# Optimization experiments

Measured on AMD Instinct MI355X. Metric: run time of the kernel, lower is better.

Reference implementation:

```python
import jax, jax.numpy as jnp
import numpy as np

B, N, DM, H, C, DC = 4, 1024, 512, 8, 3, 16  # batch, nodes, node_dim, heads, manifold components, per-component dim
DK = DM // H


def setup_inputs() -> dict:
    key = jax.random.key(0)
    ks = jax.random.split(key, 8)

    def lin_w(k):
        return jax.random.normal(k, (DM, DM), jnp.float32) / np.sqrt(DM).astype(np.float32)

    return {
        "h": jax.random.normal(ks[0], (B, N, DM), jnp.float32),
        "x": jax.random.normal(ks[1], (B, N, C * DC), jnp.float32),
        "Wq": lin_w(ks[2]), "bq": jnp.zeros((DM,), jnp.float32),
        "Wk": lin_w(ks[3]), "bk": jnp.zeros((DM,), jnp.float32),
        "Wv": lin_w(ks[4]), "bv": jnp.zeros((DM,), jnp.float32),
        "Wo": lin_w(ks[5]), "bo": jnp.zeros((DM,), jnp.float32),
        "alpha": jnp.ones((H, C), jnp.float32),
        "log_sigma": jnp.zeros((H, C), jnp.float32),
    }


def reference(h, x, Wq, bq, Wk, bk, Wv, bv, Wo, bo, alpha, log_sigma):
    b, n, dm = h.shape
    hh, cc = alpha.shape
    dk = dm // hh
    scale = 1.0 / np.sqrt(dk).astype(np.float32)

    def to_heads(t, W, bias):
        return (t @ W.T + bias).reshape(b, n, hh, dk).transpose(0, 2, 1, 3)  # (B,H,N,dk)

    Q = to_heads(h, Wq, bq)
    K = to_heads(h, Wk, bk)
    V = to_heads(h, Wv, bv)

    attn = jnp.einsum('bhid,bhjd->bhij', Q, K) * scale  # (B,H,N,N)

    # Geodesic kernel: per-component Euclidean distances on the product manifold.
    xs = x.reshape(b, n, cc, -1)                      # (B,N,C,dc)
    sq = jnp.sum(xs * xs, axis=-1)                    # (B,N,C)
    inner = jnp.einsum('bicd,bjcd->bijc', xs, xs)     # (B,N,N,C)
    d_sq = jnp.maximum(sq[:, :, None, :] + sq[:, None, :, :] - 2.0 * inner, 0.0)  # (B,N,N,C)

    sigma = jnp.clip(jnp.exp(log_sigma), 1e-4)        # (H,C)
    # exp(-d_c^2 / (2 sigma_{h,c}^2)) -> (B,H,N,N,C), then weight by alpha and sum over c
    e = jnp.exp(-d_sq[:, None] / (2.0 * (sigma ** 2)[None, :, None, None, :])).astype(attn.dtype)
    attn = attn + jnp.einsum('hc,bhijc->bhij', alpha, e)

    p = jax.nn.softmax(attn, axis=-1)
    out = jnp.einsum('bhij,bhjd->bhid', p, V)         # (B,H,N,dk)
    out = out.transpose(0, 2, 1, 3).reshape(b, n, dm)
    return out @ Wo.T + bo
```

## Files before the change

kernel.cpp:

```cpp
#include <hip/hip_runtime.h>
#include <math.h>

typedef __bf16 bf16;
typedef __attribute__((ext_vector_type(8))) __bf16 bf16x8;
typedef __attribute__((ext_vector_type(4))) float f32x4;

#define LOG2E 1.44269504088896f
#define SCALE 0.125f

__device__ inline f32x4 mfma16(bf16x8 a, bf16x8 b, f32x4 c) {
    return __builtin_amdgcn_mfma_f32_16x16x32_bf16(a, b, c, 0, 0, 0);
}
__device__ inline unsigned short bfb(bf16 v) {
    union { bf16 b; unsigned short u; } z; z.b = v; return z.u;
}

__global__ __launch_bounds__(256) void prep_kernel(
        const float* __restrict__ h, const float* __restrict__ x,
        const float* __restrict__ Wq, const float* __restrict__ Wk,
        const float* __restrict__ Wv, const float* __restrict__ Wo,
        const float* __restrict__ bq, const float* __restrict__ bk,
        const float* __restrict__ bv,
        bf16* __restrict__ hb, bf16* __restrict__ wpack, bf16* __restrict__ wob,
        float* __restrict__ bqkv, bf16* __restrict__ xb,
        unsigned* __restrict__ spack) {
    int stride = gridDim.x * blockDim.x;
    int tid = blockIdx.x * blockDim.x + threadIdx.x;
    for (int i = tid; i < 4096 * 512; i += stride) hb[i] = (bf16)h[i];
    for (int i = tid; i < 262144; i += stride) {
        wpack[i]          = (bf16)Wq[i];
        wpack[262144 + i] = (bf16)Wk[i];
        wpack[524288 + i] = (bf16)Wv[i];
    }
    for (int i = tid; i < 512 * 512; i += stride) wob[i] = (bf16)Wo[i];
    for (int i = tid; i < 1536; i += stride)
        bqkv[i] = (i < 512) ? bq[i] : (i < 1024 ? bk[i - 512] : bv[i - 1024]);
    for (int i = tid; i < 4096 * 48; i += stride) xb[i] = (bf16)x[i];
    for (int i = tid; i < 4096 * 3; i += stride) {
        int row = i / 3, c = i - row * 3;
        float s = 0.0f;
        for (int k = 0; k < 16; k++) {
            float v = (float)(bf16)x[row * 48 + c * 16 + k];
            s += v * v;
        }
        s = -0.5f * s;
        bf16 sh = (bf16)s;
        bf16 sl = (bf16)(s - (float)sh);
        spack[i] = (unsigned)bfb(sh) | ((unsigned)bfb(sl) << 16);
    }
}

__global__ __launch_bounds__(256) void gemm_qkv_kernel(
        const bf16* __restrict__ A, const bf16* __restrict__ Bm,
        const float* __restrict__ bias,
        bf16* __restrict__ Qb, bf16* __restrict__ Kb, bf16* __restrict__ Vt) {
    __shared__ bf16 smem[2 * 128 * 72];
    bf16 (*Asm)[72] = (bf16(*)[72])smem;
    bf16 (*Bsm)[72] = (bf16(*)[72])(smem + 128 * 72);
    int t = threadIdx.x, w = t >> 6, lane = t & 63, g = lane >> 4, lo = lane & 15;
    int rowbase = blockIdx.x * 128, colbase = blockIdx.y * 128;
    int wr = (w >> 1) * 64, wc = (w & 1) * 64;
    f32x4 acc[4][4] = {};
    int srow = t >> 2, scol = (t & 3) * 16;
    for (int kb = 0; kb < 512; kb += 64) {
        __syncthreads();
        for (int half = 0; half < 2; half++) {
            int r = srow + 64 * half;
            *(bf16x8*)&Asm[r][scol]     = *(const bf16x8*)&A[(size_t)(rowbase + r) * 512 + kb + scol];
            *(bf16x8*)&Asm[r][scol + 8] = *(const bf16x8*)&A[(size_t)(rowbase + r) * 512 + kb + scol + 8];
            *(bf16x8*)&Bsm[r][scol]     = *(const bf16x8*)&Bm[(size_t)(colbase + r) * 512 + kb + scol];
            *(bf16x8*)&Bsm[r][scol + 8] = *(const bf16x8*)&Bm[(size_t)(colbase + r) * 512 + kb + scol + 8];
        }
        __syncthreads();
        for (int kk = 0; kk < 64; kk += 32) {
            bf16x8 af[4], bfr[4];
            for (int m = 0; m < 4; m++) af[m]  = *(const bf16x8*)&Asm[wr + 16 * m + lo][kk + 8 * g];
            for (int n = 0; n < 4; n++) bfr[n] = *(const bf16x8*)&Bsm[wc + 16 * n + lo][kk + 8 * g];
            for (int m = 0; m < 4; m++)
                for (int n = 0; n < 4; n++)
                    acc[m][n] = mfma16(af[m], bfr[n], acc[m][n]);
        }
    }
    __syncthreads();
    bf16 (*Cl)[132] = (bf16(*)[132])smem;
    for (int n = 0; n < 4; n++) {
        float bv = bias[colbase + wc + 16 * n + lo];
        for (int m = 0; m < 4; m++)
            for (int r = 0; r < 4; r++)
                Cl[wr + 16 * m + 4 * g + r][wc + 16 * n + lo] = (bf16)(acc[m][n][r] + bv);
    }
    __syncthreads();
    int proj = colbase >> 9, h0 = (colbase >> 6) & 7;
    int bidx = rowbase >> 10, i0g = rowbase & 1023;
    if (proj < 2) {
        int row = t >> 1, half = t & 1;
        bf16* dst = (proj == 0 ? Qb : Kb) +
                    ((size_t)(bidx * 8 + h0 + half) * 1024 + i0g + row) * 64;
        for (int ch = 0; ch < 8; ch++)
            *(bf16x8*)&dst[ch * 8] = *(const bf16x8*)&Cl[row][half * 64 + ch * 8];
    } else {
        int dcol = t >> 1, ihalf = t & 1;
        int head = h0 + (dcol >> 6), d = dcol & 63;
        bf16* dst = Vt + ((size_t)(bidx * 8 + head) * 64 + d) * 1024 + i0g + ihalf * 64;
        for (int ch = 0; ch < 8; ch++) {
            bf16x8 v;
            for (int q = 0; q < 8; q++) v[q] = Cl[ihalf * 64 + ch * 8 + q][dcol];
            *(bf16x8*)&dst[ch * 8] = v;
        }
    }
}

__global__ __launch_bounds__(256) void attn_kernel(
        const bf16* __restrict__ Qb, const bf16* __restrict__ Kb,
        const bf16* __restrict__ Vt, const bf16* __restrict__ xb,
        const unsigned* __restrict__ spack,
        const float* __restrict__ alpha, const float* __restrict__ log_sigma,
        int nsplit, float* __restrict__ o_part, float* __restrict__ l_part) {
    __shared__ bf16 Klds[64][72];
    __shared__ bf16 VTlds[64][72];
    __shared__ bf16 Xlds[64][104];
    __shared__ bf16 Plds[4][16][72];

    int t = threadIdx.x;
    int w = t >> 6, lane = t & 63, g = lane >> 4, lo = lane & 15;
    int zz = blockIdx.z;
    int b = zz / nsplit, split = zz - b * nsplit;
    int hh = blockIdx.y;
    int i0 = blockIdx.x * 64 + w * 16;

    const unsigned ONE2 = 0x3F803F80u;
    float c1 = SCALE * LOG2E;
    float k2[3], alf[3];
    for (int c = 0; c < 3; c++) {
        float sg = fmaxf(expf(log_sigma[hh * 3 + c]), 1e-4f);
        k2[c] = LOG2E / (sg * sg);
        alf[c] = alpha[hh * 3 + c] * LOG2E;
    }

    const bf16* Qbase = Qb + ((size_t)(b * 8 + hh) * 1024 + i0) * 64;
    bf16x8 qa[2];
    qa[0] = *(const bf16x8*)&Qbase[lo * 64 + 8 * g];
    qa[1] = *(const bf16x8*)&Qbase[lo * 64 + 32 + 8 * g];

    bf16x8 xqa[3];
    for (int c = 0; c < 3; c++) {
        bf16x8 v = {};
        if (g < 2) {
            v = *(const bf16x8*)&xb[((size_t)(b << 10) + i0 + lo) * 48 + c * 16 + 8 * g];
        } else if (g == 2) {
            uint2 ap;
            ap.x = spack[((size_t)(b << 10) + i0 + lo) * 3 + c];
            ap.y = ONE2;
            ((uint2*)&v)[0] = ap;
        }
        xqa[c] = v;
    }

    bf16x8 ones;
    for (int e = 0; e < 8; e++) ones[e] = (bf16)1.0f;
    f32x4 o[4] = {};
    f32x4 lacc = {};

    for (int idx = t; idx < 1664; idx += 256)
        ((unsigned long long*)&Xlds[0][0])[idx] = 0ULL;

    int sr = t >> 2, sc = (t & 3) * 16;
    int jlen = 1024 / nsplit, jb = split * jlen;
    for (int j0 = jb; j0 < jb + jlen; j0 += 64) {
        __syncthreads();
        const bf16* Kbase = Kb + ((size_t)(b * 8 + hh) * 1024 + j0) * 64;
        *(bf16x8*)&Klds[sr][sc]     = *(const bf16x8*)&Kbase[sr * 64 + sc];
        *(bf16x8*)&Klds[sr][sc + 8] = *(const bf16x8*)&Kbase[sr * 64 + sc + 8];
        const bf16* Vbase = Vt + ((size_t)(b * 8 + hh) * 64) * 1024 + j0;
        *(bf16x8*)&VTlds[sr][sc]     = *(const bf16x8*)&Vbase[sr * 1024 + sc];
        *(bf16x8*)&VTlds[sr][sc + 8] = *(const bf16x8*)&Vbase[sr * 1024 + sc + 8];
        if (t < 192) {
            int xr = t / 3, c = t - xr * 3;
            const bf16* xsrc = &xb[((size_t)(b << 10) + j0 + xr) * 48 + c * 16];
            *(bf16x8*)&Xlds[xr][c * 32]     = *(const bf16x8*)&xsrc[0];
            *(bf16x8*)&Xlds[xr][c * 32 + 8] = *(const bf16x8*)&xsrc[8];
            uint2 bp;
            bp.x = ONE2;
            bp.y = spack[((size_t)(b << 10) + j0 + xr) * 3 + c];
            *(uint2*)&Xlds[xr][c * 32 + 16] = bp;
        }
        __syncthreads();

        for (int tt = 0; tt < 4; tt++) {
            f32x4 acc = {};
            bf16x8 kb0 = *(const bf16x8*)&Klds[16 * tt + lo][8 * g];
            bf16x8 kb1 = *(const bf16x8*)&Klds[16 * tt + lo][32 + 8 * g];
            acc = mfma16(qa[0], kb0, acc);
            acc = mfma16(qa[1], kb1, acc);
            f32x4 z0 = {}, z1 = {}, z2 = {};
            f32x4 e0 = mfma16(xqa[0], *(const bf16x8*)&Xlds[16 * tt + lo][8 * g], z0);
            f32x4 e1 = mfma16(xqa[1], *(const bf16x8*)&Xlds[16 * tt + lo][32 + 8 * g], z1);
            f32x4 e2 = mfma16(xqa[2], *(const bf16x8*)&Xlds[16 * tt + lo][64 + 8 * g], z2);
            for (int r = 0; r < 4; r++) {
                float t0 = alf[0] * exp2f(k2[0] * fminf(e0[r], 0.0f));
                t0 = fmaf(alf[1], exp2f(k2[1] * fminf(e1[r], 0.0f)), t0);
                t0 = fmaf(alf[2], exp2f(k2[2] * fminf(e2[r], 0.0f)), t0);
                float p = exp2f(fmaf(acc[r], c1, t0));
                Plds[w][4 * g + r][16 * tt + lo] = (bf16)p;
            }
        }

        bf16x8 pa0 = *(const bf16x8*)&Plds[w][lo][8 * g];
        bf16x8 pa1 = *(const bf16x8*)&Plds[w][lo][32 + 8 * g];
        lacc = mfma16(pa0, ones, lacc);
        lacc = mfma16(pa1, ones, lacc);
        for (int td = 0; td < 4; td++) {
            bf16x8 vb0 = *(const bf16x8*)&VTlds[16 * td + lo][8 * g];
            bf16x8 vb1 = *(const bf16x8*)&VTlds[16 * td + lo][32 + 8 * g];
            o[td] = mfma16(pa0, vb0, o[td]);
            o[td] = mfma16(pa1, vb1, o[td]);
        }
    }

    for (int td = 0; td < 4; td++)
        for (int r = 0; r < 4; r++) {
            size_t rowg = (size_t)(b * 8 + hh) * 1024 + i0 + 4 * g + r;
            o_part[((size_t)split * 32768 + rowg) * 64 + 16 * td + lo] = o[td][r];
        }
    if (lo == 0)
        for (int r = 0; r < 4; r++) {
            size_t rowg = (size_t)(b * 8 + hh) * 1024 + i0 + 4 * g + r;
            l_part[(size_t)split * 32768 + rowg] = lacc[r];
        }
}

__global__ __launch_bounds__(256) void merge_kernel(
        const float* __restrict__ o_part, const float* __restrict__ l_part,
        int nsplit, bf16* __restrict__ attnout) {
    int t = threadIdx.x;
    int rowg = blockIdx.x * 16 + (t >> 4);
    int d4 = (t & 15) * 4;
    float l = l_part[rowg];
    f32x4 a = *(const f32x4*)&o_part[(size_t)rowg * 64 + d4];
    if (nsplit == 2) {
        l += l_part[32768 + rowg];
        f32x4 b2 = *(const f32x4*)&o_part[((size_t)32768 + rowg) * 64 + d4];
        for (int q = 0; q < 4; q++) a[q] += b2[q];
    }
    float inv = 1.0f / l;
    int b = rowg >> 13, hh = (rowg >> 10) & 7, i = rowg & 1023;
    bf16* dst = &attnout[((size_t)(b << 10) + i) * 512 + hh * 64 + d4];
    for (int q = 0; q < 4; q++) dst[q] = (bf16)(a[q] * inv);
}

__global__ __launch_bounds__(256) void gemm_out_kernel(
        const bf16* __restrict__ A, const bf16* __restrict__ Bm,
        const float* __restrict__ bias, float* __restrict__ out) {
    __shared__ bf16 smem[2 * 128 * 72];
    bf16 (*Asm)[72] = (bf16(*)[72])smem;
    bf16 (*Bsm)[72] = (bf16(*)[72])(smem + 128 * 72);
    int t = threadIdx.x, w = t >> 6, lane = t & 63, g = lane >> 4, lo = lane & 15;
    int rowbase = blockIdx.x * 128, colbase = blockIdx.y * 128;
    int wr = (w >> 1) * 64, wc = (w & 1) * 64;
    f32x4 acc[4][4] = {};
    int srow = t >> 2, scol = (t & 3) * 16;
    for (int kb = 0; kb < 512; kb += 64) {
        __syncthreads();
        for (int half = 0; half < 2; half++) {
            int r = srow + 64 * half;
            *(bf16x8*)&Asm[r][scol]     = *(const bf16x8*)&A[(size_t)(rowbase + r) * 512 + kb + scol];
            *(bf16x8*)&Asm[r][scol + 8] = *(const bf16x8*)&A[(size_t)(rowbase + r) * 512 + kb + scol + 8];
            *(bf16x8*)&Bsm[r][scol]     = *(const bf16x8*)&Bm[(size_t)(colbase + r) * 512 + kb + scol];
            *(bf16x8*)&Bsm[r][scol + 8] = *(const bf16x8*)&Bm[(size_t)(colbase + r) * 512 + kb + scol + 8];
        }
        __syncthreads();
        for (int kk = 0; kk < 64; kk += 32) {
            bf16x8 af[4], bfr[4];
            for (int m = 0; m < 4; m++) af[m]  = *(const bf16x8*)&Asm[wr + 16 * m + lo][kk + 8 * g];
            for (int n = 0; n < 4; n++) bfr[n] = *(const bf16x8*)&Bsm[wc + 16 * n + lo][kk + 8 * g];
            for (int m = 0; m < 4; m++)
                for (int n = 0; n < 4; n++)
                    acc[m][n] = mfma16(af[m], bfr[n], acc[m][n]);
        }
    }
    for (int n = 0; n < 4; n++) {
        int mcol = colbase + wc + 16 * n + lo;
        float bv = bias[mcol];
        for (int m = 0; m < 4; m++)
            for (int r = 0; r < 4; r++)
                out[(size_t)(rowbase + wr + 16 * m + 4 * g + r) * 512 + mcol] =
                    acc[m][n][r] + bv;
    }
}

extern "C" void kernel_launch(void* const* d_in, const int* in_sizes, int n_in,
                              void* d_out, int out_size, void* d_ws, size_t ws_size,
                              hipStream_t stream) {
    const float* h  = (const float*)d_in[0];
    const float* x  = (const float*)d_in[1];
    const float* Wq = (const float*)d_in[2];
    const float* bq = (const float*)d_in[3];
    const float* Wk = (const float*)d_in[4];
    const float* bk = (const float*)d_in[5];
    const float* Wv = (const float*)d_in[6];
    const float* bv = (const float*)d_in[7];
    const float* Wo = (const float*)d_in[8];
    const float* bo = (const float*)d_in[9];
    const float* alpha     = (const float*)d_in[10];
    const float* log_sigma = (const float*)d_in[11];
    float* out = (float*)d_out;

    char* ws = (char*)d_ws;
    size_t off = 0;
    auto alloc = [&](size_t bytes) {
        char* p = ws + off;
        off += (bytes + 255) & ~(size_t)255;
        return p;
    };
    bf16*     hb      = (bf16*)alloc(4096 * 512 * 2);
    bf16*     wpack   = (bf16*)alloc(1536 * 512 * 2);
    bf16*     wob     = (bf16*)alloc(512 * 512 * 2);
    float*    bqkv    = (float*)alloc(1536 * 4);
    bf16*     xb      = (bf16*)alloc(4096 * 48 * 2);
    unsigned* spack   = (unsigned*)alloc((size_t)4096 * 3 * 4);
    bf16*     Qb      = (bf16*)alloc((size_t)4 * 8 * 1024 * 64 * 2);
    bf16*     Kb      = (bf16*)alloc((size_t)4 * 8 * 1024 * 64 * 2);
    bf16*     Vt      = (bf16*)alloc((size_t)4 * 8 * 1024 * 64 * 2);
    bf16*     attnout = (bf16*)alloc(4096 * 512 * 2);
    size_t base = off;

    size_t need2 = base + 2 * ((size_t)32768 * 64 * 4 + 1024) + 2 * ((size_t)32768 * 4 + 1024);
    int nsplit = (ws_size >= need2) ? 2 : 1;
    float* o_part = (float*)alloc((size_t)nsplit * 32768 * 64 * 4);
    float* l_part = (float*)alloc((size_t)nsplit * 32768 * 4);

    prep_kernel<<<512, 256, 0, stream>>>(h, x, Wq, Wk, Wv, Wo, bq, bk, bv,
                                         hb, wpack, wob, bqkv, xb, spack);
    gemm_qkv_kernel<<<dim3(32, 12), 256, 0, stream>>>(hb, wpack, bqkv, Qb, Kb, Vt);
    attn_kernel<<<dim3(16, 8, 4 * nsplit), 256, 0, stream>>>(
        Qb, Kb, Vt, xb, spack, alpha, log_sigma, nsplit, o_part, l_part);
    merge_kernel<<<2048, 256, 0, stream>>>(o_part, l_part, nsplit, attnout);
    gemm_out_kernel<<<dim3(32, 4), 256, 0, stream>>>(attnout, wob, bo, out);
}
```

Before: 172.6 us.

## Drop split-KV merge, normalize in attention epilogue, vectorize prep, shrink out-GEMM tile

Removes the two-way KV split and separate merge kernel so each attention block covers all keys and writes normalized bf16 output directly. Prep conversions are vectorized to float4 loads and 8-wide bf16 stores. The output GEMM uses 64-row tiles, doubling the grid. This cuts a launch and fp32 partial traffic, but halves attention grid parallelism.

```diff
diff --git a/kernel.cpp b/kernel.cpp
--- a/kernel.cpp
+++ b/kernel.cpp
@@ -13,6 +13,12 @@
 }
 __device__ inline unsigned short bfb(bf16 v) {
     union { bf16 b; unsigned short u; } z; z.b = v; return z.u;
+}
+__device__ inline bf16x8 cvt8(float4 v0, float4 v1) {
+    bf16x8 o;
+    o[0] = (bf16)v0.x; o[1] = (bf16)v0.y; o[2] = (bf16)v0.z; o[3] = (bf16)v0.w;
+    o[4] = (bf16)v1.x; o[5] = (bf16)v1.y; o[6] = (bf16)v1.z; o[7] = (bf16)v1.w;
+    return o;
 }
 
 __global__ __launch_bounds__(256) void prep_kernel(
@@ -26,16 +32,26 @@
         unsigned* __restrict__ spack) {
     int stride = gridDim.x * blockDim.x;
     int tid = blockIdx.x * blockDim.x + threadIdx.x;
-    for (int i = tid; i < 4096 * 512; i += stride) hb[i] = (bf16)h[i];
     for (int i = tid; i < 262144; i += stride) {
-        wpack[i]          = (bf16)Wq[i];
-        wpack[262144 + i] = (bf16)Wk[i];
-        wpack[524288 + i] = (bf16)Wv[i];
-    }
-    for (int i = tid; i < 512 * 512; i += stride) wob[i] = (bf16)Wo[i];
+        const float4* s = (const float4*)h + 2 * i;
+        ((bf16x8*)hb)[i] = cvt8(s[0], s[1]);
+    }
+    for (int i = tid; i < 32768; i += stride) {
+        const float4* sq = (const float4*)Wq + 2 * i;
+        const float4* sk = (const float4*)Wk + 2 * i;
+        const float4* sv = (const float4*)Wv + 2 * i;
+        const float4* so = (const float4*)Wo + 2 * i;
+        ((bf16x8*)wpack)[i]         = cvt8(sq[0], sq[1]);
+        ((bf16x8*)wpack)[32768 + i] = cvt8(sk[0], sk[1]);
+        ((bf16x8*)wpack)[65536 + i] = cvt8(sv[0], sv[1]);
+        ((bf16x8*)wob)[i]           = cvt8(so[0], so[1]);
+    }
+    for (int i = tid; i < 24576; i += stride) {
+        const float4* s = (const float4*)x + 2 * i;
+        ((bf16x8*)xb)[i] = cvt8(s[0], s[1]);
+    }
     for (int i = tid; i < 1536; i += stride)
         bqkv[i] = (i < 512) ? bq[i] : (i < 1024 ? bk[i - 512] : bv[i - 1024]);
-    for (int i = tid; i < 4096 * 48; i += stride) xb[i] = (bf16)x[i];
     for (int i = tid; i < 4096 * 3; i += stride) {
         int row = i / 3, c = i - row * 3;
         float s = 0.0f;
@@ -115,7 +131,7 @@
         const bf16* __restrict__ Vt, const bf16* __restrict__ xb,
         const unsigned* __restrict__ spack,
         const float* __restrict__ alpha, const float* __restrict__ log_sigma,
-        int nsplit, float* __restrict__ o_part, float* __restrict__ l_part) {
+        bf16* __restrict__ attnout) {
     __shared__ bf16 Klds[64][72];
     __shared__ bf16 VTlds[64][72];
     __shared__ bf16 Xlds[64][104];
@@ -123,8 +139,7 @@
 
     int t = threadIdx.x;
     int w = t >> 6, lane = t & 63, g = lane >> 4, lo = lane & 15;
-    int zz = blockIdx.z;
-    int b = zz / nsplit, split = zz - b * nsplit;
+    int b = blockIdx.z;
     int hh = blockIdx.y;
     int i0 = blockIdx.x * 64 + w * 16;
 
@@ -165,8 +180,7 @@
         ((unsigned long long*)&Xlds[0][0])[idx] = 0ULL;
 
     int sr = t >> 2, sc = (t & 3) * 16;
-    int jlen = 1024 / nsplit, jb = split * jlen;
-    for (int j0 = jb; j0 < jb + jlen; j0 += 64) {
+    for (int j0 = 0; j0 < 1024; j0 += 64) {
         __syncthreads();
         const bf16* Kbase = Kb + ((size_t)(b * 8 + hh) * 1024 + j0) * 64;
         *(bf16x8*)&Klds[sr][sc]     = *(const bf16x8*)&Kbase[sr * 64 + sc];
@@ -217,63 +231,41 @@
         }
     }
 
+    float inv[4];
+    for (int r = 0; r < 4; r++) inv[r] = 1.0f / lacc[r];
     for (int td = 0; td < 4; td++)
         for (int r = 0; r < 4; r++) {
-            size_t rowg = (size_t)(b * 8 + hh) * 1024 + i0 + 4 * g + r;
-            o_part[((size_t)split * 32768 + rowg) * 64 + 16 * td + lo] = o[td][r];
-        }
-    if (lo == 0)
-        for (int r = 0; r < 4; r++) {
-            size_t rowg = (size_t)(b * 8 + hh) * 1024 + i0 + 4 * g + r;
-            l_part[(size_t)split * 32768 + rowg] = lacc[r];
-        }
-}
-
-__global__ __launch_bounds__(256) void merge_kernel(
-        const float* __restrict__ o_part, const float* __restrict__ l_part,
-        int nsplit, bf16* __restrict__ attnout) {
-    int t = threadIdx.x;
-    int rowg = blockIdx.x * 16 + (t >> 4);
-    int d4 = (t & 15) * 4;
-    float l = l_part[rowg];
-    f32x4 a = *(const f32x4*)&o_part[(size_t)rowg * 64 + d4];
-    if (nsplit == 2) {
-        l += l_part[32768 + rowg];
-        f32x4 b2 = *(const f32x4*)&o_part[((size_t)32768 + rowg) * 64 + d4];
-        for (int q = 0; q < 4; q++) a[q] += b2[q];
-    }
-    float inv = 1.0f / l;
-    int b = rowg >> 13, hh = (rowg >> 10) & 7, i = rowg & 1023;
-    bf16* dst = &attnout[((size_t)(b << 10) + i) * 512 + hh * 64 + d4];
-    for (int q = 0; q < 4; q++) dst[q] = (bf16)(a[q] * inv);
+            int i = i0 + 4 * g + r;
+            attnout[((size_t)(b << 10) + i) * 512 + hh * 64 + 16 * td + lo] =
+                (bf16)(o[td][r] * inv[r]);
+        }
 }
 
 __global__ __launch_bounds__(256) void gemm_out_kernel(
         const bf16* __restrict__ A, const bf16* __restrict__ Bm,
         const float* __restrict__ bias, float* __restrict__ out) {
-    __shared__ bf16 smem[2 * 128 * 72];
-    bf16 (*Asm)[72] = (bf16(*)[72])smem;
-    bf16 (*Bsm)[72] = (bf16(*)[72])(smem + 128 * 72);
+    __shared__ bf16 Asm[64][72];
+    __shared__ bf16 Bsm[128][72];
     int t = threadIdx.x, w = t >> 6, lane = t & 63, g = lane >> 4, lo = lane & 15;
-    int rowbase = blockIdx.x * 128, colbase = blockIdx.y * 128;
-    int wr = (w >> 1) * 64, wc = (w & 1) * 64;
-    f32x4 acc[4][4] = {};
-    int srow = t >> 2, scol = (t & 3) * 16;
+    int rowbase = blockIdx.x * 64, colbase = blockIdx.y * 128;
+    int wr = (w >> 1) * 32, wc = (w & 1) * 64;
+    f32x4 acc[2][4] = {};
+    int arow = t >> 2, acol = (t & 3) * 16;
+    int brow = t >> 1, bcol = (t & 1) * 32;
     for (int kb = 0; kb < 512; kb += 64) {
         __syncthreads();
-        for (int half = 0; half < 2; half++) {
-            int r = srow + 64 * half;
-            *(bf16x8*)&Asm[r][scol]     = *(const bf16x8*)&A[(size_t)(rowbase + r) * 512 + kb + scol];
-            *(bf16x8*)&Asm[r][scol + 8] = *(const bf16x8*)&A[(size_t)(rowbase + r) * 512 + kb + scol + 8];
-            *(bf16x8*)&Bsm[r][scol]     = *(const bf16x8*)&Bm[(size_t)(colbase + r) * 512 + kb + scol];
-            *(bf16x8*)&Bsm[r][scol + 8] = *(const bf16x8*)&Bm[(size_t)(colbase + r) * 512 + kb + scol + 8];
-        }
+        *(bf16x8*)&Asm[arow][acol]     = *(const bf16x8*)&A[(size_t)(rowbase + arow) * 512 + kb + acol];
+        *(bf16x8*)&Asm[arow][acol + 8] = *(const bf16x8*)&A[(size_t)(rowbase + arow) * 512 + kb + acol + 8];
+        *(bf16x8*)&Bsm[brow][bcol]      = *(const bf16x8*)&Bm[(size_t)(colbase + brow) * 512 + kb + bcol];
+        *(bf16x8*)&Bsm[brow][bcol + 8]  = *(const bf16x8*)&Bm[(size_t)(colbase + brow) * 512 + kb + bcol + 8];
+        *(bf16x8*)&Bsm[brow][bcol + 16] = *(const bf16x8*)&Bm[(size_t)(colbase + brow) * 512 + kb + bcol + 16];
+        *(bf16x8*)&Bsm[brow][bcol + 24] = *(const bf16x8*)&Bm[(size_t)(colbase + brow) * 512 + kb + bcol + 24];
         __syncthreads();
         for (int kk = 0; kk < 64; kk += 32) {
-            bf16x8 af[4], bfr[4];
-            for (int m = 0; m < 4; m++) af[m]  = *(const bf16x8*)&Asm[wr + 16 * m + lo][kk + 8 * g];
+            bf16x8 af[2], bfr[4];
+            for (int m = 0; m < 2; m++) af[m]  = *(const bf16x8*)&Asm[wr + 16 * m + lo][kk + 8 * g];
             for (int n = 0; n < 4; n++) bfr[n] = *(const bf16x8*)&Bsm[wc + 16 * n + lo][kk + 8 * g];
-            for (int m = 0; m < 4; m++)
+            for (int m = 0; m < 2; m++)
                 for (int n = 0; n < 4; n++)
                     acc[m][n] = mfma16(af[m], bfr[n], acc[m][n]);
         }
@@ -281,7 +273,7 @@
     for (int n = 0; n < 4; n++) {
         int mcol = colbase + wc + 16 * n + lo;
         float bv = bias[mcol];
-        for (int m = 0; m < 4; m++)
+        for (int m = 0; m < 2; m++)
             for (int r = 0; r < 4; r++)
                 out[(size_t)(rowbase + wr + 16 * m + 4 * g + r) * 512 + mcol] =
                     acc[m][n][r] + bv;
@@ -322,18 +314,11 @@
     bf16*     Kb      = (bf16*)alloc((size_t)4 * 8 * 1024 * 64 * 2);
     bf16*     Vt      = (bf16*)alloc((size_t)4 * 8 * 1024 * 64 * 2);
     bf16*     attnout = (bf16*)alloc(4096 * 512 * 2);
-    size_t base = off;
-
-    size_t need2 = base + 2 * ((size_t)32768 * 64 * 4 + 1024) + 2 * ((size_t)32768 * 4 + 1024);
-    int nsplit = (ws_size >= need2) ? 2 : 1;
-    float* o_part = (float*)alloc((size_t)nsplit * 32768 * 64 * 4);
-    float* l_part = (float*)alloc((size_t)nsplit * 32768 * 4);
 
     prep_kernel<<<512, 256, 0, stream>>>(h, x, Wq, Wk, Wv, Wo, bq, bk, bv,
                                          hb, wpack, wob, bqkv, xb, spack);
     gemm_qkv_kernel<<<dim3(32, 12), 256, 0, stream>>>(hb, wpack, bqkv, Qb, Kb, Vt);
-    attn_kernel<<<dim3(16, 8, 4 * nsplit), 256, 0, stream>>>(
-        Qb, Kb, Vt, xb, spack, alpha, log_sigma, nsplit, o_part, l_part);
-    merge_kernel<<<2048, 256, 0, stream>>>(o_part, l_part, nsplit, attnout);
-    gemm_out_kernel<<<dim3(32, 4), 256, 0, stream>>>(attnout, wob, bo, out);
-}
+    attn_kernel<<<dim3(16, 8, 4), 256, 0, stream>>>(
+        Qb, Kb, Vt, xb, spack, alpha, log_sigma, attnout);
+    gemm_out_kernel<<<dim3(64, 4), 256, 0, stream>>>(attnout, wob, bo, out);
+}
```

New measurement: 171.3 us. Within noise of the previous version (-0.7%).
